# Kernel optimization log

Hardware: AMD Instinct MI355X
Metric: run time of the kernel (lower is better)

Reference implementation:

```python
import jax, jax.numpy as jnp
import numpy as np
from jax import lax

C_EDGE, C_DVS, C_OUT = 128, 128, 128
H, W = 32, 32
MASK_SIZE = 7
THRESH, TAU, GAMA = 1.0, 0.5, 1.0  # LIFSpike defaults (ZIF surrogate)


def _window_mask(h, w, mask_size):
    half = mask_size // 2
    qx = jnp.arange(h)[:, None, None, None]
    qy = jnp.arange(w)[None, :, None, None]
    kx = jnp.arange(h)[None, None, :, None]
    ky = jnp.arange(w)[None, None, None, :]
    allowed = (jnp.abs(kx - qx) <= half) & (jnp.abs(ky - qy) <= half)
    return jnp.where(allowed, 0.0, -10000.0).reshape(h * w, h * w).astype(jnp.float32)


@jax.custom_vjp
def _spike(x):
    return (x > 0).astype(x.dtype)

def _spike_fwd(x):
    return _spike(x), x

def _spike_bwd(x, g):
    # ZIF surrogate: grad = clamp(gama - |x|, 0) / gama^2
    return (g * jnp.clip(GAMA - jnp.abs(x), 0.0, None) / (GAMA * GAMA),)

_spike.defvjp(_spike_fwd, _spike_bwd)


def _lif(x):
    # x: (B, T, C, H, W) -> spikes, scan over time
    xt = jnp.moveaxis(x, 1, 0)  # (T, B, C, H, W)

    def step(mem, inp):
        mem = mem * TAU + inp
        spk = _spike(mem - THRESH)
        mem = (1.0 - spk) * mem
        return mem, spk

    _, spikes = lax.scan(step, jnp.zeros_like(xt[0]), xt)
    return jnp.moveaxis(spikes, 0, 1)


def setup_inputs() -> dict:
    key = jax.random.key(0)
    ks = jax.random.split(key, 16)
    s = 0.05
    return {
        "edge_features": jax.random.normal(ks[0], (8, 4, C_EDGE, H, W), jnp.float32),
        "dvs_features": jax.random.normal(ks[1], (8, 4, C_DVS, H, W), jnp.float32),
        "We": jax.random.normal(ks[2], (C_OUT, C_EDGE), jnp.float32) * s,
        "be": jax.random.normal(ks[3], (C_OUT,), jnp.float32) * s,
        "Wd": jax.random.normal(ks[4], (C_OUT, C_DVS), jnp.float32) * s,
        "bd": jax.random.normal(ks[5], (C_OUT,), jnp.float32) * s,
        "Wq": jax.random.normal(ks[6], (C_OUT, C_OUT), jnp.float32) * s,
        "bq": jax.random.normal(ks[7], (C_OUT,), jnp.float32) * s,
        "Wk": jax.random.normal(ks[8], (C_OUT, C_OUT), jnp.float32) * s,
        "bk": jax.random.normal(ks[9], (C_OUT,), jnp.float32) * s,
        "Wv": jax.random.normal(ks[10], (C_OUT, C_OUT), jnp.float32) * s,
        "bv": jax.random.normal(ks[11], (C_OUT,), jnp.float32) * s,
        "Wf": jax.random.normal(ks[12], (C_OUT, C_OUT), jnp.float32) * s,
        "bf": jax.random.normal(ks[13], (C_OUT,), jnp.float32) * s,
    }


def reference(edge_features, dvs_features, We, be, Wd, bd, Wq, bq, Wk, bk, Wv, bv, Wf, bf):
    B, T, _, h, w = dvs_features.shape
    C = We.shape[0]
    N = h * w
    # 1x1 conv channel alignment (SeqToANNContainer folds B,T)
    ef = (jnp.einsum('btchw,oc->btohw', edge_features, We) + be[None, None, :, None, None]).reshape(B * T, C, h, w)
    df = (jnp.einsum('btchw,oc->btohw', dvs_features, Wd) + bd[None, None, :, None, None]).reshape(B * T, C, h, w)
    # cosine similarity over channels
    l2e = jnp.sqrt(jnp.sum(ef * ef, axis=1, keepdims=True))
    l2d = jnp.sqrt(jnp.sum(df * df, axis=1, keepdims=True))
    sim = jnp.sum((ef / (l2e + 1e-6)) * (df / (l2d + 1e-6)), axis=1, keepdims=True)
    sim = (sim + 1.0) * 0.5
    # density: softmax of edge L2 norm over spatial, scaled by N
    dens = (jax.nn.softmax(l2e.reshape(B * T, N), axis=1) * N).reshape(B * T, 1, h, w)
    ew = (ef * sim).reshape(B * T, C, N)
    dw = (df * dens).reshape(B * T, C, N)
    # conv1d k=1 Q/K/V projections
    q = jnp.einsum('oc,bcn->bon', Wq, ew) + bq[None, :, None]
    k = jnp.einsum('oc,bcn->bon', Wk, dw) + bk[None, :, None]
    v = jnp.einsum('oc,bcn->bon', Wv, dw) + bv[None, :, None]
    mask = _window_mask(h, w, MASK_SIZE)
    attn = jnp.einsum('bcq,bck->bqk', q, k) / (C ** 0.5) + mask[None]
    attn = jax.nn.softmax(attn, axis=-1)
    out = jnp.einsum('bqk,bck->bqc', attn, v)  # (BT, N, C)
    out = out.reshape(B * T, h, w, C).transpose(0, 3, 1, 2).reshape(B, T, C, h, w)
    fused = jnp.einsum('btchw,oc->btohw', out, Wf) + bf[None, None, :, None, None]
    return _lif(fused)
```

## Files before the change

kernel.cpp:

```cpp
#include <hip/hip_runtime.h>
#include <math.h>

#define CC 128
#define NN 1024
#define BTOT 32
#define CP 152
#define PSTs 40
#define CPA 136
#define CQS 36

typedef unsigned short u16;
typedef u16 u16x8 __attribute__((ext_vector_type(8)));
typedef u16 u16x4 __attribute__((ext_vector_type(4)));
typedef __bf16 bf16x8 __attribute__((ext_vector_type(8)));
typedef float f32x4 __attribute__((ext_vector_type(4)));

__device__ __forceinline__ u16 f2b(float f) {
    unsigned int u = __float_as_uint(f);
    u += 0x7FFFu + ((u >> 16) & 1u);
    return (u16)(u >> 16);
}
__device__ __forceinline__ float b2f(u16 u) {
    return __uint_as_float(((unsigned int)u) << 16);
}

__device__ __forceinline__ void loadB(const u16* brow, int g, bf16x8 bfr[4]) {
#pragma unroll
    for (int kk = 0; kk < 4; ++kk)
        bfr[kk] = *(const bf16x8*)(brow + kk * 32 + g * 8);
}
__device__ __forceinline__ bf16x8 ldA(const u16* __restrict__ WB, int ot, int kk, int l) {
    return *(const bf16x8*)(WB + ((size_t)(ot * 4 + kk) * 64 + l) * 8);
}

__global__ __launch_bounds__(256) void k_prep(
    const float* __restrict__ We, const float* __restrict__ Wd,
    const float* __restrict__ Wf, const float* __restrict__ Wq,
    const float* __restrict__ Wk, const float* __restrict__ Wv,
    const float* __restrict__ be, const float* __restrict__ bd,
    u16* __restrict__ out, float* __restrict__ cvec)
{
    const int bid = blockIdx.x, t = threadIdx.x;
    if (bid < 24) {
        const int gid = bid * 256 + t;
        const int wi = gid >> 11;
        const float* W = (wi == 0) ? We : (wi == 1) ? Wd : Wf;
        const int slot = (wi == 2) ? 5 : wi;
        const int rem = gid & 2047;
        const int ot = rem >> 8, kk = (rem >> 6) & 3, l = rem & 63;
        const int row = ot * 16 + (l & 15), col = kk * 32 + (l >> 4) * 8;
        float4 a = *(const float4*)(W + row * CC + col);
        float4 b = *(const float4*)(W + row * CC + col + 4);
        u16x8 u;
        u[0] = f2b(a.x); u[1] = f2b(a.y); u[2] = f2b(a.z); u[3] = f2b(a.w);
        u[4] = f2b(b.x); u[5] = f2b(b.y); u[6] = f2b(b.z); u[7] = f2b(b.w);
        *(u16x8*)(out + (size_t)slot * 16384 + ((size_t)(ot * 4 + kk) * 64 + l) * 8) = u;
    } else {
        const int cid = bid - 24;
        const int mat = cid >> 6;
        const int o = ((cid & 63) << 1) | (t >> 7);
        const int c = t & 127;
        const float* A = (mat == 0) ? Wq : (mat == 1) ? Wk : Wv;
        const float* B = (mat == 0) ? We : Wd;
        const float* bvec = (mat == 0) ? be : bd;
        float acc = 0.f;
        for (int m = 0; m < CC; ++m) acc += A[o * CC + m] * B[m * CC + c];
        const int ot = o >> 4, l15o = o & 15;
        const int kk = c >> 5, gc = (c >> 3) & 3, j = c & 7;
        const int l = gc * 16 + l15o;
        out[(size_t)(2 + mat) * 16384 + ((size_t)(ot * 4 + kk) * 64 + l) * 8 + j] = f2b(acc);
        if (c == 0) {
            float bacc = 0.f;
            for (int m = 0; m < CC; ++m) bacc += A[o * CC + m] * bvec[m];
            cvec[mat * CC + o] = bacc;
        }
    }
}

__global__ __launch_bounds__(256) void k_front(
    const float* __restrict__ edge, const float* __restrict__ dvs,
    const u16* __restrict__ WeB, const u16* __restrict__ WdB,
    const u16* __restrict__ WqeB, const u16* __restrict__ WkdB,
    const u16* __restrict__ WvdB,
    const float* __restrict__ be, const float* __restrict__ bd,
    const float* __restrict__ bq,
    const float* __restrict__ cq, const float* __restrict__ ck,
    const float* __restrict__ cv,
    float* __restrict__ l2e_out,
    u16* __restrict__ qT, u16* __restrict__ kT, u16* __restrict__ vN)
{
    __shared__ u16 bufA[64 * CP];
    __shared__ u16 bufB[64 * CP];
    const int t = threadIdx.x;
    const int id = blockIdx.x;
    const int bt = (id & 7) * 4 + ((id >> 3) & 3);
    const int n0b = (id >> 5) * 64;
    const float* eb = edge + (size_t)bt * CC * NN + n0b;
    const float* db = dvs + (size_t)bt * CC * NN + n0b;

#pragma unroll
    for (int j = 0; j < 2; ++j) {
        const int i = t + 256 * j;
        const int c4 = i >> 4, p = i & 15;
        float4 e[4], d[4];
#pragma unroll
        for (int m = 0; m < 4; ++m) {
            e[m] = *(const float4*)(eb + (size_t)(4 * c4 + m) * NN + 4 * p);
            d[m] = *(const float4*)(db + (size_t)(4 * c4 + m) * NN + 4 * p);
        }
#pragma unroll
        for (int n = 0; n < 4; ++n) {
            u16x4 ue, ud;
            ue[0] = f2b(((const float*)&e[0])[n]); ud[0] = f2b(((const float*)&d[0])[n]);
            ue[1] = f2b(((const float*)&e[1])[n]); ud[1] = f2b(((const float*)&d[1])[n]);
            ue[2] = f2b(((const float*)&e[2])[n]); ud[2] = f2b(((const float*)&d[2])[n]);
            ue[3] = f2b(((const float*)&e[3])[n]); ud[3] = f2b(((const float*)&d[3])[n]);
            *(u16x4*)&bufA[(4 * p + n) * CP + 4 * c4] = ue;
            *(u16x4*)&bufB[(4 * p + n) * CP + 4 * c4] = ud;
        }
    }
    __syncthreads();

    const int w = t >> 6, l = t & 63;
    const int l15 = l & 15, g = l >> 4;
    const int nloc = w * 16 + l15;
    const size_t gn = (size_t)bt * NN + n0b + nloc;

    bf16x8 bfrE[4], bfrD[4];
    loadB(bufA + nloc * CP, g, bfrE);
    loadB(bufB + nloc * CP, g, bfrD);

    f32x4 aE[8], aD[8];
#pragma unroll
    for (int ot = 0; ot < 8; ++ot) {
        aE[ot] = *(const f32x4*)(be + 16 * ot + 4 * g);
        aD[ot] = *(const f32x4*)(bd + 16 * ot + 4 * g);
    }
#pragma unroll
    for (int ot = 0; ot < 8; ++ot)
#pragma unroll
        for (int kk = 0; kk < 4; ++kk) {
            aE[ot] = __builtin_amdgcn_mfma_f32_16x16x32_bf16(ldA(WeB, ot, kk, l), bfrE[kk], aE[ot], 0, 0, 0);
            aD[ot] = __builtin_amdgcn_mfma_f32_16x16x32_bf16(ldA(WdB, ot, kk, l), bfrD[kk], aD[ot], 0, 0, 0);
        }
    float s2e = 0.f, s2d = 0.f, sed = 0.f;
#pragma unroll
    for (int ot = 0; ot < 8; ++ot)
#pragma unroll
        for (int r = 0; r < 4; ++r) {
            const float fe = aE[ot][r], fd = aD[ot][r];
            s2e += fe * fe; s2d += fd * fd; sed += fe * fd;
        }
    s2e += __shfl_xor(s2e, 16); s2e += __shfl_xor(s2e, 32);
    s2d += __shfl_xor(s2d, 16); s2d += __shfl_xor(s2d, 32);
    sed += __shfl_xor(sed, 16); sed += __shfl_xor(sed, 32);
    const float le = sqrtf(s2e), ld = sqrtf(s2d);
    const float sim = (sed / ((le + 1e-6f) * (ld + 1e-6f)) + 1.0f) * 0.5f;
    if (g == 0) l2e_out[gn] = le;

    {
        f32x4 aQ[8];
#pragma unroll
        for (int ot = 0; ot < 8; ++ot) aQ[ot] = *(const f32x4*)(cq + 16 * ot + 4 * g);
#pragma unroll
        for (int ot = 0; ot < 8; ++ot)
#pragma unroll
            for (int kk = 0; kk < 4; ++kk)
                aQ[ot] = __builtin_amdgcn_mfma_f32_16x16x32_bf16(ldA(WqeB, ot, kk, l), bfrE[kk], aQ[ot], 0, 0, 0);
#pragma unroll
        for (int ot = 0; ot < 8; ++ot) {
            f32x4 b4 = *(const f32x4*)(bq + 16 * ot + 4 * g);
            u16x4 u;
#pragma unroll
            for (int r = 0; r < 4; ++r) u[r] = f2b(sim * aQ[ot][r] + b4[r]);
            *(u16x4*)(qT + gn * CC + 16 * ot + 4 * g) = u;
        }
    }
    {
        f32x4 aK[8];
#pragma unroll
        for (int ot = 0; ot < 8; ++ot) aK[ot] = *(const f32x4*)(ck + 16 * ot + 4 * g);
#pragma unroll
        for (int ot = 0; ot < 8; ++ot)
#pragma unroll
            for (int kk = 0; kk < 4; ++kk)
                aK[ot] = __builtin_amdgcn_mfma_f32_16x16x32_bf16(ldA(WkdB, ot, kk, l), bfrD[kk], aK[ot], 0, 0, 0);
#pragma unroll
        for (int ot = 0; ot < 8; ++ot) {
            u16x4 u;
#pragma unroll
            for (int r = 0; r < 4; ++r) u[r] = f2b(aK[ot][r]);
            *(u16x4*)(kT + gn * CC + 16 * ot + 4 * g) = u;
        }
    }
    {
        f32x4 aV[8];
#pragma unroll
        for (int ot = 0; ot < 8; ++ot) aV[ot] = *(const f32x4*)(cv + 16 * ot + 4 * g);
#pragma unroll
        for (int ot = 0; ot < 8; ++ot)
#pragma unroll
            for (int kk = 0; kk < 4; ++kk)
                aV[ot] = __builtin_amdgcn_mfma_f32_16x16x32_bf16(ldA(WvdB, ot, kk, l), bfrD[kk], aV[ot], 0, 0, 0);
        __syncthreads();
        u16* bufT = bufA;
#pragma unroll
        for (int ot = 0; ot < 8; ++ot)
#pragma unroll
            for (int r = 0; r < 4; ++r)
                bufT[(16 * ot + 4 * g + r) * 72 + nloc] = f2b(aV[ot][r]);
        __syncthreads();
#pragma unroll
        for (int p = 0; p < 4; ++p) {
            const int idx = t + 256 * p;
            const int c = idx >> 3, n8 = (idx & 7) * 8;
            *(u16x8*)(vN + ((size_t)bt * CC + c) * NN + n0b + n8) =
                *(const u16x8*)&bufT[c * 72 + n8];
        }
    }
}

__global__ __launch_bounds__(256) void k_dens(const float* __restrict__ l2e,
                                              float* __restrict__ dens)
{
    __shared__ float red1[4];
    __shared__ float red2[4];
    const int bt = blockIdx.x, t = threadIdx.x;
    const int lane = t & 63, wid = t >> 6;
    const float* x = l2e + (size_t)bt * NN;
    float v[4], m = -1e30f;
#pragma unroll
    for (int i = 0; i < 4; ++i) { v[i] = x[t + 256 * i]; m = fmaxf(m, v[i]); }
#pragma unroll
    for (int off = 32; off >= 1; off >>= 1) m = fmaxf(m, __shfl_xor(m, off));
    if (lane == 0) red1[wid] = m;
    __syncthreads();
    m = fmaxf(fmaxf(red1[0], red1[1]), fmaxf(red1[2], red1[3]));
    float e[4], s = 0.f;
#pragma unroll
    for (int i = 0; i < 4; ++i) { e[i] = expf(v[i] - m); s += e[i]; }
#pragma unroll
    for (int off = 32; off >= 1; off >>= 1) s += __shfl_xor(s, off);
    if (lane == 0) red2[wid] = s;
    __syncthreads();
    s = red2[0] + red2[1] + red2[2] + red2[3];
    const float scale = 1024.0f / s;
#pragma unroll
    for (int i = 0; i < 4; ++i) dens[(size_t)bt * NN + t + 256 * i] = e[i] * scale;
}

__global__ __launch_bounds__(256) void k_attnf(
    const u16* __restrict__ qT, const u16* __restrict__ kT,
    const u16* __restrict__ vN, const float* __restrict__ dens,
    const float* __restrict__ bk, const float* __restrict__ bv,
    const u16* __restrict__ WfB, const float* __restrict__ bf,
    float* __restrict__ out)
{
    __shared__ u16 lds_u16[26624];
    const int t = threadIdx.x;
    const int id = blockIdx.x;
    const int b = id & 7, qx = id >> 3;
    const int w = t >> 6;
    const int bt = b * 4 + w;
    const int l = t & 63, l15 = l & 15, g = l >> 4;
    u16* att = lds_u16;
    float* convq = (float*)(lds_u16 + 17408);
    u16* P = lds_u16 + w * 32 * PSTs;
    const size_t btNN = (size_t)bt * NN;
    const float invsq = 0.08838834764831843f;

    u16x8 ql[2][4];
#pragma unroll
    for (int nt = 0; nt < 2; ++nt)
#pragma unroll
        for (int kk = 0; kk < 4; ++kk)
            ql[nt][kk] = *(const u16x8*)(qT + (btNN + qx * 32 + 16 * nt + l15) * CC + 32 * kk + 8 * g);

    float qbk[2] = {0.f, 0.f};
#pragma unroll
    for (int kk = 0; kk < 4; ++kk) {
        f32x4 b0 = *(const f32x4*)(bk + 32 * kk + 8 * g);
        f32x4 b1 = *(const f32x4*)(bk + 32 * kk + 8 * g + 4);
#pragma unroll
        for (int nt = 0; nt < 2; ++nt)
#pragma unroll
            for (int j = 0; j < 4; ++j) {
                qbk[nt] += b2f(ql[nt][kk][j]) * b0[j];
                qbk[nt] += b2f(ql[nt][kk][4 + j]) * b1[j];
            }
    }
#pragma unroll
    for (int nt = 0; nt < 2; ++nt) {
        qbk[nt] += __shfl_xor(qbk[nt], 16);
        qbk[nt] += __shfl_xor(qbk[nt], 32);
    }

    float ssum[2] = {0.f, 0.f};
    f32x4 o[8][2];
#pragma unroll
    for (int mt = 0; mt < 8; ++mt)
#pragma unroll
        for (int nt = 0; nt < 2; ++nt) o[mt][nt] = (f32x4){0.f, 0.f, 0.f, 0.f};

#pragma unroll
    for (int i = 0; i < 7; ++i) {
        const int kxr = qx - 3 + i;
        const int kxc = min(max(kxr, 0), 31);
        const bool cval = (kxr == kxc);
        f32x4 acc[2][2];
#pragma unroll
        for (int mt = 0; mt < 2; ++mt)
#pragma unroll
            for (int nt = 0; nt < 2; ++nt) acc[mt][nt] = (f32x4){0.f, 0.f, 0.f, 0.f};
#pragma unroll
        for (int kk = 0; kk < 4; ++kk)
#pragma unroll
            for (int mt = 0; mt < 2; ++mt) {
                bf16x8 ka = *(const bf16x8*)(kT + (btNN + kxc * 32 + 16 * mt + l15) * CC + 32 * kk + 8 * g);
#pragma unroll
                for (int nt = 0; nt < 2; ++nt)
                    acc[mt][nt] = __builtin_amdgcn_mfma_f32_16x16x32_bf16(
                        ka, __builtin_bit_cast(bf16x8, ql[nt][kk]), acc[mt][nt], 0, 0, 0);
            }
#pragma unroll
        for (int mt = 0; mt < 2; ++mt) {
            f32x4 d4 = *(const f32x4*)(dens + btNN + kxc * 32 + 16 * mt + 4 * g);
#pragma unroll
            for (int nt = 0; nt < 2; ++nt) {
                const int qyv = l15 + 16 * nt;
                u16x4 pw;
#pragma unroll
                for (int r = 0; r < 4; ++r) {
                    const float s = (d4[r] * acc[mt][nt][r] + qbk[nt]) * invsq;
                    const int ky = 16 * mt + 4 * g + r;
                    const int dy = ky - qyv;
                    const bool vld = cval && (dy >= -3) && (dy <= 3);
                    const float e = vld ? __expf(s) : 0.f;
                    ssum[nt] += e;
                    pw[r] = f2b(e * d4[r]);
                }
                *(u16x4*)&P[qyv * PSTs + 16 * mt + 4 * g] = pw;
            }
        }
        asm volatile("s_waitcnt lgkmcnt(0)" ::: "memory");
        __builtin_amdgcn_sched_barrier(0);
        bf16x8 pb[2];
#pragma unroll
        for (int nt = 0; nt < 2; ++nt)
            pb[nt] = *(const bf16x8*)&P[(16 * nt + l15) * PSTs + 8 * g];
#pragma unroll
        for (int mt = 0; mt < 8; ++mt) {
            bf16x8 va = *(const bf16x8*)(vN + ((size_t)bt * CC + 16 * mt + l15) * NN + kxc * 32 + 8 * g);
#pragma unroll
            for (int nt = 0; nt < 2; ++nt)
                o[mt][nt] = __builtin_amdgcn_mfma_f32_16x16x32_bf16(va, pb[nt], o[mt][nt], 0, 0, 0);
        }
    }
    float inv[2];
#pragma unroll
    for (int nt = 0; nt < 2; ++nt) {
        float s = ssum[nt];
        s += __shfl_xor(s, 16);
        s += __shfl_xor(s, 32);
        inv[nt] = 1.0f / s;
    }

    __syncthreads();

    u16* attw = att + w * 32 * CPA;
#pragma unroll
    for (int mt = 0; mt < 8; ++mt) {
        f32x4 bv4 = *(const f32x4*)(bv + 16 * mt + 4 * g);
#pragma unroll
        for (int nt = 0; nt < 2; ++nt) {
            u16x4 ov;
#pragma unroll
            for (int r = 0; r < 4; ++r) ov[r] = f2b(o[mt][nt][r] * inv[nt] + bv4[r]);
            *(u16x4*)&attw[(16 * nt + l15) * CPA + 16 * mt + 4 * g] = ov;
        }
    }
    asm volatile("s_waitcnt lgkmcnt(0)" ::: "memory");
    __builtin_amdgcn_sched_barrier(0);

    bf16x8 cb[4][2];
#pragma unroll
    for (int kk = 0; kk < 4; ++kk)
#pragma unroll
        for (int nt = 0; nt < 2; ++nt)
            cb[kk][nt] = *(const bf16x8*)&attw[(16 * nt + l15) * CPA + 32 * kk + 8 * g];

    const int cl = t >> 3, n4 = (t & 7) * 4;
#pragma unroll
    for (int cr = 0; cr < 4; ++cr) {
#pragma unroll
        for (int oi = 0; oi < 2; ++oi) {
            const int ot = 2 * cr + oi;
            f32x4 ca[2];
#pragma unroll
            for (int nt = 0; nt < 2; ++nt) ca[nt] = *(const f32x4*)(bf + 16 * ot + 4 * g);
#pragma unroll
            for (int kk = 0; kk < 4; ++kk) {
                bf16x8 afr = ldA(WfB, ot, kk, l);
#pragma unroll
                for (int nt = 0; nt < 2; ++nt)
                    ca[nt] = __builtin_amdgcn_mfma_f32_16x16x32_bf16(afr, cb[kk][nt], ca[nt], 0, 0, 0);
            }
#pragma unroll
            for (int nt = 0; nt < 2; ++nt)
#pragma unroll
                for (int r = 0; r < 4; ++r)
                    convq[w * 32 * CQS + (16 * oi + 4 * g + r) * CQS + 16 * nt + l15] = ca[nt][r];
        }
        __syncthreads();
        f32x4 mem = {0.f, 0.f, 0.f, 0.f};
#pragma unroll
        for (int tt = 0; tt < 4; ++tt) {
            f32x4 x = *(const f32x4*)&convq[tt * 32 * CQS + cl * CQS + n4];
            f32x4 mv = mem * 0.5f + x;
            float4 sp;
            sp.x = (mv[0] > 1.0f) ? 1.0f : 0.0f; if (mv[0] > 1.0f) mv[0] = 0.f;
            sp.y = (mv[1] > 1.0f) ? 1.0f : 0.0f; if (mv[1] > 1.0f) mv[1] = 0.f;
            sp.z = (mv[2] > 1.0f) ? 1.0f : 0.0f; if (mv[2] > 1.0f) mv[2] = 0.f;
            sp.w = (mv[3] > 1.0f) ? 1.0f : 0.0f; if (mv[3] > 1.0f) mv[3] = 0.f;
            *(float4*)(out + ((size_t)(b * 4 + tt) * CC + 32 * cr + cl) * NN + qx * 32 + n4) = sp;
            mem = mv;
        }
        __syncthreads();
    }
}

extern "C" void kernel_launch(void* const* d_in, const int* in_sizes, int n_in,
                              void* d_out, int out_size, void* d_ws, size_t ws_size,
                              hipStream_t stream) {
    (void)in_sizes; (void)n_in; (void)out_size; (void)ws_size;
    const float* edge = (const float*)d_in[0];
    const float* dvs  = (const float*)d_in[1];
    const float* We = (const float*)d_in[2];
    const float* be = (const float*)d_in[3];
    const float* Wd = (const float*)d_in[4];
    const float* bd = (const float*)d_in[5];
    const float* Wq = (const float*)d_in[6];
    const float* bq = (const float*)d_in[7];
    const float* Wk = (const float*)d_in[8];
    const float* bk = (const float*)d_in[9];
    const float* Wv = (const float*)d_in[10];
    const float* bv = (const float*)d_in[11];
    const float* Wf = (const float*)d_in[12];
    const float* bf = (const float*)d_in[13];
    float* out = (float*)d_out;

    const size_t S = (size_t)BTOT * NN * CC;
    u16* qT   = (u16*)d_ws;
    u16* kT   = qT + S;
    u16* vN   = kT + S;
    u16* WbAll = vN + S;
    float* fbase = (float*)(WbAll + 6 * 16384);
    float* cvec  = fbase;
    float* l2e   = cvec + 3 * CC;
    float* dens  = l2e + BTOT * NN;
    u16* WeB  = WbAll + 0 * 16384;
    u16* WdB  = WbAll + 1 * 16384;
    u16* WqeB = WbAll + 2 * 16384;
    u16* WkdB = WbAll + 3 * 16384;
    u16* WvdB = WbAll + 4 * 16384;
    u16* WfB  = WbAll + 5 * 16384;
    float* cq = cvec;
    float* ck = cvec + CC;
    float* cv = cvec + 2 * CC;

    k_prep<<<216, 256, 0, stream>>>(We, Wd, Wf, Wq, Wk, Wv, be, bd, WbAll, cvec);
    k_front<<<512, 256, 0, stream>>>(edge, dvs, WeB, WdB, WqeB, WkdB, WvdB,
                                     be, bd, bq, cq, ck, cv, l2e, qT, kT, vN);
    k_dens<<<BTOT, 256, 0, stream>>>(l2e, dens);
    k_attnf<<<256, 256, 0, stream>>>(qT, kT, vN, dens, bk, bv, WfB, bf, out);
}
```

Before: 67.97 us.

## Fold density softmax into front and attention kernels, drop k_dens launch

Removes the separate density-softmax kernel. The front kernel now writes exp(l2 norm) per pixel and a per-block partial sum, and the attention kernel sums the 16 partials and scales the exponentials on the fly. This removes one kernel launch and the l2e/dens round trip through memory. It drops the max-subtraction, so it relies on the edge L2 norms being small enough that exp does not overflow.

```diff
diff --git a/kernel.cpp b/kernel.cpp
--- a/kernel.cpp
+++ b/kernel.cpp
@@ -86,11 +86,12 @@
     const float* __restrict__ bq,
     const float* __restrict__ cq, const float* __restrict__ ck,
     const float* __restrict__ cv,
-    float* __restrict__ l2e_out,
+    float* __restrict__ eexp_out, float* __restrict__ partial,
     u16* __restrict__ qT, u16* __restrict__ kT, u16* __restrict__ vN)
 {
     __shared__ u16 bufA[64 * CP];
     __shared__ u16 bufB[64 * CP];
+    __shared__ float redp[4];
     const int t = threadIdx.x;
     const int id = blockIdx.x;
     const int bt = (id & 7) * 4 + ((id >> 3) & 3);
@@ -156,7 +157,14 @@
     sed += __shfl_xor(sed, 16); sed += __shfl_xor(sed, 32);
     const float le = sqrtf(s2e), ld = sqrtf(s2d);
     const float sim = (sed / ((le + 1e-6f) * (ld + 1e-6f)) + 1.0f) * 0.5f;
-    if (g == 0) l2e_out[gn] = le;
+    const float ee = __expf(le);
+    if (g == 0) eexp_out[gn] = ee;
+    {
+        float s = ee;
+        s += __shfl_xor(s, 1); s += __shfl_xor(s, 2);
+        s += __shfl_xor(s, 4); s += __shfl_xor(s, 8);
+        if (l == 0) redp[w] = s;
+    }
 
     {
         f32x4 aQ[8];
@@ -203,6 +211,8 @@
             for (int kk = 0; kk < 4; ++kk)
                 aV[ot] = __builtin_amdgcn_mfma_f32_16x16x32_bf16(ldA(WvdB, ot, kk, l), bfrD[kk], aV[ot], 0, 0, 0);
         __syncthreads();
+        if (t == 0)
+            partial[(size_t)bt * 16 + (id >> 5)] = redp[0] + redp[1] + redp[2] + redp[3];
         u16* bufT = bufA;
 #pragma unroll
         for (int ot = 0; ot < 8; ++ot)
@@ -220,38 +230,10 @@
     }
 }
 
-__global__ __launch_bounds__(256) void k_dens(const float* __restrict__ l2e,
-                                              float* __restrict__ dens)
-{
-    __shared__ float red1[4];
-    __shared__ float red2[4];
-    const int bt = blockIdx.x, t = threadIdx.x;
-    const int lane = t & 63, wid = t >> 6;
-    const float* x = l2e + (size_t)bt * NN;
-    float v[4], m = -1e30f;
-#pragma unroll
-    for (int i = 0; i < 4; ++i) { v[i] = x[t + 256 * i]; m = fmaxf(m, v[i]); }
-#pragma unroll
-    for (int off = 32; off >= 1; off >>= 1) m = fmaxf(m, __shfl_xor(m, off));
-    if (lane == 0) red1[wid] = m;
-    __syncthreads();
-    m = fmaxf(fmaxf(red1[0], red1[1]), fmaxf(red1[2], red1[3]));
-    float e[4], s = 0.f;
-#pragma unroll
-    for (int i = 0; i < 4; ++i) { e[i] = expf(v[i] - m); s += e[i]; }
-#pragma unroll
-    for (int off = 32; off >= 1; off >>= 1) s += __shfl_xor(s, off);
-    if (lane == 0) red2[wid] = s;
-    __syncthreads();
-    s = red2[0] + red2[1] + red2[2] + red2[3];
-    const float scale = 1024.0f / s;
-#pragma unroll
-    for (int i = 0; i < 4; ++i) dens[(size_t)bt * NN + t + 256 * i] = e[i] * scale;
-}
-
 __global__ __launch_bounds__(256) void k_attnf(
     const u16* __restrict__ qT, const u16* __restrict__ kT,
-    const u16* __restrict__ vN, const float* __restrict__ dens,
+    const u16* __restrict__ vN, const float* __restrict__ eexp,
+    const float* __restrict__ partial,
     const float* __restrict__ bk, const float* __restrict__ bv,
     const u16* __restrict__ WfB, const float* __restrict__ bf,
     float* __restrict__ out)
@@ -269,6 +251,14 @@
     const size_t btNN = (size_t)bt * NN;
     const float invsq = 0.08838834764831843f;
 
+    float S = 0.f;
+    {
+        const float* pp = partial + (size_t)bt * 16;
+#pragma unroll
+        for (int i = 0; i < 16; ++i) S += pp[i];
+    }
+    const float dscale = 1024.0f / S;
+
     u16x8 ql[2][4];
 #pragma unroll
     for (int nt = 0; nt < 2; ++nt)
@@ -324,7 +314,10 @@
             }
 #pragma unroll
         for (int mt = 0; mt < 2; ++mt) {
-            f32x4 d4 = *(const f32x4*)(dens + btNN + kxc * 32 + 16 * mt + 4 * g);
+            f32x4 ee4 = *(const f32x4*)(eexp + btNN + kxc * 32 + 16 * mt + 4 * g);
+            f32x4 d4;
+#pragma unroll
+            for (int r = 0; r < 4; ++r) d4[r] = dscale * ee4[r];
 #pragma unroll
             for (int nt = 0; nt < 2; ++nt) {
                 const int qyv = l15 + 16 * nt;
@@ -456,8 +449,8 @@
     u16* WbAll = vN + S;
     float* fbase = (float*)(WbAll + 6 * 16384);
     float* cvec  = fbase;
-    float* l2e   = cvec + 3 * CC;
-    float* dens  = l2e + BTOT * NN;
+    float* eexp  = cvec + 3 * CC;
+    float* partial = eexp + BTOT * NN;
     u16* WeB  = WbAll + 0 * 16384;
     u16* WdB  = WbAll + 1 * 16384;
     u16* WqeB = WbAll + 2 * 16384;
@@ -470,7 +463,6 @@
 
     k_prep<<<216, 256, 0, stream>>>(We, Wd, Wf, Wq, Wk, Wv, be, bd, WbAll, cvec);
     k_front<<<512, 256, 0, stream>>>(edge, dvs, WeB, WdB, WqeB, WkdB, WvdB,
-                                     be, bd, bq, cq, ck, cv, l2e, qT, kT, vN);
-    k_dens<<<BTOT, 256, 0, stream>>>(l2e, dens);
-    k_attnf<<<256, 256, 0, stream>>>(qT, kT, vN, dens, bk, bv, WfB, bf, out);
-}
+                                     be, bd, bq, cq, ck, cv, eexp, partial, qT, kT, vN);
+    k_attnf<<<256, 256, 0, stream>>>(qT, kT, vN, eexp, partial, bk, bv, WfB, bf, out);
+}
```

New measurement: 64.92 us, median of 2. -4.5%, faster.
